# Optimization experiments

Measured on AMD Instinct MI355X. Metric: run time of the kernel, lower is better.

The kernel has to match this reference:

```python
import jax, jax.numpy as jnp
import numpy as np

B, S, D = 2, 2048, 1024
H = 16
DH = D // H  # 64


def setup_inputs() -> dict:
    key = jax.random.key(0)
    ks = jax.random.split(key, 7)
    q = jax.random.normal(ks[0], (B, S, D), dtype=jnp.float32)
    k = jax.random.normal(ks[1], (B, S, D), dtype=jnp.float32)
    v = jax.random.normal(ks[2], (B, S, D), dtype=jnp.float32)
    # torch.rand -> uniform[0,1)
    w_q = jax.random.uniform(ks[3], (D, D), dtype=jnp.float32)
    w_k = jax.random.uniform(ks[4], (DH, D), dtype=jnp.float32)
    w_v = jax.random.uniform(ks[5], (DH, D), dtype=jnp.float32)
    w_out = jax.random.uniform(ks[6], (D, D), dtype=jnp.float32)
    return {"q": q, "k": k, "v": v, "w_q": w_q, "w_k": w_k, "w_v": w_v, "w_out": w_out}


def reference(q, k, v, w_q, w_k, w_v, w_out):
    # F.linear(x, W) = x @ W.T
    qp = jnp.einsum('bsd,ed->bse', q, w_q)          # [B,S,D]
    kp = jnp.einsum('bsd,hd->bsh', k, w_k)          # [B,S,DH] shared K head
    vp = jnp.einsum('bsd,hd->bsh', v, w_v)          # [B,S,DH] shared V head
    qh = qp.reshape(B, S, H, DH).transpose(0, 2, 1, 3)  # [B,H,S,DH]
    scale = 1.0 / jnp.sqrt(jnp.float32(DH))
    scores = jnp.einsum('bhsd,btd->bhst', qh, kp) * scale  # [B,H,S,S]
    attn = jax.nn.softmax(scores, axis=-1)
    out = jnp.einsum('bhst,btd->bhsd', attn, vp)    # [B,H,S,DH]
    out = out.transpose(0, 2, 1, 3).reshape(B, S, D)
    return jnp.einsum('bsd,ed->bse', out, w_out)
```

## Files before the change

kernel.cpp:

```cpp
#include <hip/hip_runtime.h>
#include <hip/hip_bf16.h>
#include <stdint.h>


#define B_   2
#define S_   2048
#define D_   1024
#define H_   16
#define DH_  64
#define MTOT (B_ * S_)
#define NSPL 4

typedef short bf16x8 __attribute__((ext_vector_type(8)));
typedef float f32x4 __attribute__((ext_vector_type(4)));
typedef float f32x16 __attribute__((ext_vector_type(16)));
typedef short short4v __attribute__((ext_vector_type(4)));
typedef unsigned uint4v __attribute__((ext_vector_type(4)));

__device__ __forceinline__ short f2bf(float f) {
  unsigned u = __float_as_uint(f);
  u += 0x7FFF + ((u >> 16) & 1);
  return (short)(u >> 16);
}
__device__ __forceinline__ float bf2f(short h) {
  return __uint_as_float(((unsigned)(unsigned short)h) << 16);
}
struct bfpair { short hi, lo; };
__device__ __forceinline__ bfpair split2(float x) {
  bfpair p;
  p.hi = f2bf(x);
  p.lo = f2bf(x - bf2f(p.hi));
  return p;
}
__device__ __forceinline__ unsigned cvtpk(float lo, float hi) {
  unsigned r;
  asm("v_cvt_pk_bf16_f32 %0, %1, %2" : "=v"(r) : "v"(lo), "v"(hi));
  return r;
}

__device__ __forceinline__ void glds16(const void* g, void* l) {
  __builtin_amdgcn_global_load_lds((const __attribute__((address_space(1))) void*)g,
                                   (__attribute__((address_space(3))) void*)l, 16, 0, 0);
}

__global__ __launch_bounds__(256) void cvt_split(
    const float* __restrict__ q, const float* __restrict__ k, const float* __restrict__ v,
    const float* __restrict__ wq, const float* __restrict__ wk, const float* __restrict__ wv,
    const float* __restrict__ wo,
    short* qhi, short* qlo, short* khi, short* klo, short* vb,
    short* wqh, short* wql, short* wkh, short* wkl, short* wvb,
    short* woh, short* wol) {
  const int U0 = 1048576, U1 = 2097152, U2 = 3145728, U3 = 3407872,
            U4 = 3424256, U5 = 3440640, U6 = 3702784;
  for (int u = blockIdx.x * blockDim.x + threadIdx.x; u < U6; u += gridDim.x * blockDim.x) {
    const float* s; short* dh; short* dl; int r;
    if (u < U0)      { s = q;  dh = qhi; dl = qlo; r = u; }
    else if (u < U1) { s = k;  dh = khi; dl = klo; r = u - U0; }
    else if (u < U2) { s = v;  dh = vb;  dl = nullptr; r = u - U1; }
    else if (u < U3) { s = wq; dh = wqh; dl = wql; r = u - U2; }
    else if (u < U4) { s = wk; dh = wkh; dl = wkl; r = u - U3; }
    else if (u < U5) { s = wv; dh = wvb; dl = nullptr; r = u - U4; }
    else             { s = wo; dh = woh; dl = wol; r = u - U5; }
    float4 x = *(const float4*)(s + (size_t)r * 4);
    bfpair p0 = split2(x.x), p1 = split2(x.y), p2 = split2(x.z), p3 = split2(x.w);
    short4v yh, yl;
    yh.x = p0.hi; yh.y = p1.hi; yh.z = p2.hi; yh.w = p3.hi;
    yl.x = p0.lo; yl.y = p1.lo; yl.z = p2.lo; yl.w = p3.lo;
    *(short4v*)(dh + (size_t)r * 4) = yh;
    if (dl) *(short4v*)(dl + (size_t)r * 4) = yl;
  }
}

template <int NPROD, int MODE>
__global__ __launch_bounds__(256) void gemm3(
    const short* __restrict__ Ah, const short* __restrict__ Al,
    const short* __restrict__ Bh, const short* __restrict__ Bl,
    short* __restrict__ Ch, short* __restrict__ Cl, float* __restrict__ Cf,
    int K, int lda, int ldb, int ldc, float alpha) {
  __shared__ alignas(16) short Ash[4096], Asl[4096], Bsh[4096], Bsl[4096];
  const int tid = threadIdx.x;
  const int lane = tid & 63, w = tid >> 6;
  const int c = lane & 15, g = lane >> 4;
  const int wm = w >> 1, wn = w & 1;
  const int bm = blockIdx.x * 64, bn = blockIdx.y * 64;
  const int sr = lane >> 3;
  const int scs = ((lane & 7) ^ sr) * 8;

  f32x4 acc[2][2] = {};
  for (int k0 = 0; k0 < K; k0 += 64) {
    glds16(Ah + (size_t)(bm + w * 8 + sr) * lda + k0 + scs,      Ash + w * 512);
    glds16(Ah + (size_t)(bm + 32 + w * 8 + sr) * lda + k0 + scs, Ash + 2048 + w * 512);
    glds16(Bh + (size_t)(bn + w * 8 + sr) * ldb + k0 + scs,      Bsh + w * 512);
    glds16(Bh + (size_t)(bn + 32 + w * 8 + sr) * ldb + k0 + scs, Bsh + 2048 + w * 512);
    if constexpr (NPROD == 3) {
      glds16(Al + (size_t)(bm + w * 8 + sr) * lda + k0 + scs,      Asl + w * 512);
      glds16(Al + (size_t)(bm + 32 + w * 8 + sr) * lda + k0 + scs, Asl + 2048 + w * 512);
      glds16(Bl + (size_t)(bn + w * 8 + sr) * ldb + k0 + scs,      Bsl + w * 512);
      glds16(Bl + (size_t)(bn + 32 + w * 8 + sr) * ldb + k0 + scs, Bsl + 2048 + w * 512);
    }
    __syncthreads();
#pragma unroll
    for (int kk = 0; kk < 2; ++kk) {
      bf16x8 ah[2], bh[2], al[2], bl[2];
#pragma unroll
      for (int mt = 0; mt < 2; ++mt) {
        int row = wm * 32 + mt * 16 + c;
        int so = row * 64 + (((kk * 4 + g) ^ (row & 7)) * 8);
        ah[mt] = *(const bf16x8*)(Ash + so);
        if constexpr (NPROD == 3) al[mt] = *(const bf16x8*)(Asl + so);
      }
#pragma unroll
      for (int nt = 0; nt < 2; ++nt) {
        int row = wn * 32 + nt * 16 + c;
        int so = row * 64 + (((kk * 4 + g) ^ (row & 7)) * 8);
        bh[nt] = *(const bf16x8*)(Bsh + so);
        if constexpr (NPROD == 3) bl[nt] = *(const bf16x8*)(Bsl + so);
      }
#pragma unroll
      for (int mt = 0; mt < 2; ++mt)
#pragma unroll
        for (int nt = 0; nt < 2; ++nt) {
          acc[mt][nt] = __builtin_amdgcn_mfma_f32_16x16x32_bf16(ah[mt], bh[nt], acc[mt][nt], 0, 0, 0);
          if constexpr (NPROD == 3) {
            acc[mt][nt] = __builtin_amdgcn_mfma_f32_16x16x32_bf16(ah[mt], bl[nt], acc[mt][nt], 0, 0, 0);
            acc[mt][nt] = __builtin_amdgcn_mfma_f32_16x16x32_bf16(al[mt], bh[nt], acc[mt][nt], 0, 0, 0);
          }
        }
    }
    __syncthreads();
  }
#pragma unroll
  for (int mt = 0; mt < 2; ++mt) {
#pragma unroll
    for (int nt = 0; nt < 2; ++nt) {
#pragma unroll
      for (int r = 0; r < 4; ++r) {
        int m = bm + wm * 32 + mt * 16 + g * 4 + r;
        int n = bn + wn * 32 + nt * 16 + c;
        float val = acc[mt][nt][r] * alpha;
        if constexpr (MODE == 0) {
          bfpair pr = split2(val);
          Ch[(size_t)m * ldc + n] = pr.hi;
          Cl[(size_t)m * ldc + n] = pr.lo;
        } else if constexpr (MODE == 3) {
          Cf[(size_t)m * ldc + n] = val;
        } else if constexpr (MODE == 4) {
          size_t off = (((size_t)(m >> 5) * 4 + (n >> 4)) * 64 +
                        ((m & 31) + 32 * ((n >> 3) & 1))) * 8 + (n & 7);
          bfpair pr = split2(val);
          Ch[off] = pr.hi;
          Cl[off] = pr.lo;
        } else {
          size_t off = ((((size_t)(m >> 5) * 2 + (n >> 5)) * 2 + ((m >> 4) & 1)) * 64 +
                        ((n & 31) + 32 * ((m >> 3) & 1))) * 8 + (m & 7);
          Ch[off] = f2bf(val);
        }
      }
    }
  }
}

__global__ __launch_bounds__(256) void mqa_attn(
    const short* __restrict__ qph, const short* __restrict__ qpl,
    const short* __restrict__ pkh, const short* __restrict__ pkl,
    const short* __restrict__ pv, short* __restrict__ pO, float* __restrict__ pML) {
  const int tid = threadIdx.x;
  const int lane = tid & 63, w = tid >> 6;
  const int j = lane & 31, b5 = lane >> 5;
  const int qt = blockIdx.x, h = blockIdx.y;
  const int b = blockIdx.z >> 2, sp = blockIdx.z & 3;
  const int q0 = qt * 128 + w * 32;
  const int kvbeg = sp * (S_ / NSPL), kvend = kvbeg + S_ / NSPL;

  const size_t qbase = (size_t)(b * S_ + q0 + j) * D_ + h * DH_ + b5 * 8;
  bf16x8 qh[4], ql[4];
#pragma unroll
  for (int m = 0; m < 4; ++m) {
    qh[m] = *(const bf16x8*)(qph + qbase + m * 16);
    ql[m] = *(const bf16x8*)(qpl + qbase + m * 16);
  }

  float mrow = -1.0e30f, lrow = 0.f;
  f32x16 o0 = {}, o1 = {};

  for (int kv0 = kvbeg; kv0 < kvend; kv0 += 32) {
    const size_t tg = (size_t)((b * S_ + kv0) >> 5);
    const short* kb = pkh + tg * 2048 + lane * 8;
    const short* kb2 = pkl + tg * 2048 + lane * 8;
    bf16x8 kh[4], kl[4];
#pragma unroll
    for (int m = 0; m < 4; ++m) {
      kh[m] = *(const bf16x8*)(kb + m * 512);
      kl[m] = *(const bf16x8*)(kb2 + m * 512);
    }
    f32x16 sa = {}, sb = {}, sc2 = {};
#pragma unroll
    for (int m = 0; m < 4; ++m) {
      sa  = __builtin_amdgcn_mfma_f32_32x32x16_bf16(kh[m], qh[m], sa, 0, 0, 0);
      sb  = __builtin_amdgcn_mfma_f32_32x32x16_bf16(kl[m], qh[m], sb, 0, 0, 0);
      sc2 = __builtin_amdgcn_mfma_f32_32x32x16_bf16(kh[m], ql[m], sc2, 0, 0, 0);
    }
    f32x16 s = (sa + sb) + sc2;
    float mx = s[0];
#pragma unroll
    for (int r = 1; r < 16; ++r) mx = fmaxf(mx, s[r]);
    mx = fmaxf(mx, __shfl_xor(mx, 32));
    if (!__all(mx - mrow <= 8.0f)) {
      float mn = fmaxf(mrow, mx);
      float scale = exp2f(mrow - mn);
      mrow = mn;
      lrow *= scale;
      o0 *= scale;
      o1 *= scale;
    }
    float p[16];
#pragma unroll
    for (int r = 0; r < 16; ++r) p[r] = exp2f(s[r] - mrow);
    float rs = (((p[0] + p[1]) + (p[2] + p[3])) + ((p[4] + p[5]) + (p[6] + p[7]))) +
               (((p[8] + p[9]) + (p[10] + p[11])) + ((p[12] + p[13]) + (p[14] + p[15])));
    rs += __shfl_xor(rs, 32);
    lrow += rs;
    auto r0 = __builtin_amdgcn_permlane32_swap(cvtpk(p[0], p[1]),   cvtpk(p[4], p[5]),   false, false);
    auto r1 = __builtin_amdgcn_permlane32_swap(cvtpk(p[2], p[3]),   cvtpk(p[6], p[7]),   false, false);
    auto r2 = __builtin_amdgcn_permlane32_swap(cvtpk(p[8], p[9]),   cvtpk(p[12], p[13]), false, false);
    auto r3 = __builtin_amdgcn_permlane32_swap(cvtpk(p[10], p[11]), cvtpk(p[14], p[15]), false, false);
    union { uint4v u; bf16x8 v; } pa0, pa1;
    pa0.u = (uint4v){r0[0], r1[0], r0[1], r1[1]};
    pa1.u = (uint4v){r2[0], r3[0], r2[1], r3[1]};
    const short* vbp = pv + tg * 2048 + lane * 8;
    bf16x8 va00 = *(const bf16x8*)(vbp);
    bf16x8 va01 = *(const bf16x8*)(vbp + 512);
    bf16x8 va10 = *(const bf16x8*)(vbp + 1024);
    bf16x8 va11 = *(const bf16x8*)(vbp + 1536);
    o0 = __builtin_amdgcn_mfma_f32_32x32x16_bf16(va00, pa0.v, o0, 0, 0, 0);
    o0 = __builtin_amdgcn_mfma_f32_32x32x16_bf16(va01, pa1.v, o0, 0, 0, 0);
    o1 = __builtin_amdgcn_mfma_f32_32x32x16_bf16(va10, pa0.v, o1, 0, 0, 0);
    o1 = __builtin_amdgcn_mfma_f32_32x32x16_bf16(va11, pa1.v, o1, 0, 0, 0);
  }
  const size_t tok = (size_t)(b * S_ + q0 + j);
  const size_t obase = ((size_t)sp * MTOT + tok) * D_ + h * DH_;
#pragma unroll
  for (int r = 0; r < 16; ++r) {
    int dh0 = (r & 3) + 8 * (r >> 2) + 4 * b5;
    pO[obase + dh0] = f2bf(o0[r]);
    pO[obase + 32 + dh0] = f2bf(o1[r]);
  }
  if (b5 == 0) {
    size_t mb = (((size_t)sp * MTOT + tok) * H_ + h) * 2;
    pML[mb] = mrow;
    pML[mb + 1] = lrow;
  }
}

__global__ __launch_bounds__(256) void attn_merge(
    const short* __restrict__ pO, const float* __restrict__ pML,
    short* __restrict__ aoh, short* __restrict__ aol) {
  int qd = blockIdx.x * 256 + threadIdx.x;
  size_t idx = (size_t)qd * 4;
  int tok = (int)(idx >> 10);
  int h = (int)((idx >> 6) & 15);
  float ms[NSPL], ls[NSPL], mm = -1.0e30f;
#pragma unroll
  for (int s = 0; s < NSPL; ++s) {
    size_t mb = (((size_t)s * MTOT + tok) * H_ + h) * 2;
    ms[s] = pML[mb];
    ls[s] = pML[mb + 1];
    mm = fmaxf(mm, ms[s]);
  }
  float num[4] = {}, den = 0.f;
#pragma unroll
  for (int s = 0; s < NSPL; ++s) {
    float e = exp2f(ms[s] - mm);
    den += ls[s] * e;
    short4v o4 = *(const short4v*)(pO + (size_t)s * MTOT * D_ + idx);
    num[0] += bf2f(o4.x) * e;
    num[1] += bf2f(o4.y) * e;
    num[2] += bf2f(o4.z) * e;
    num[3] += bf2f(o4.w) * e;
  }
  float inv = 1.0f / den;
  short4v yh, yl;
  bfpair p0 = split2(num[0] * inv), p1 = split2(num[1] * inv),
         p2 = split2(num[2] * inv), p3 = split2(num[3] * inv);
  yh.x = p0.hi; yh.y = p1.hi; yh.z = p2.hi; yh.w = p3.hi;
  yl.x = p0.lo; yl.y = p1.lo; yl.z = p2.lo; yl.w = p3.lo;
  *(short4v*)(aoh + idx) = yh;
  *(short4v*)(aol + idx) = yl;
}

extern "C" void kernel_launch(void* const* d_in, const int* in_sizes, int n_in,
                              void* d_out, int out_size, void* d_ws, size_t ws_size,
                              hipStream_t stream) {
  const float* q  = (const float*)d_in[0];
  const float* k  = (const float*)d_in[1];
  const float* v  = (const float*)d_in[2];
  const float* wq = (const float*)d_in[3];
  const float* wk = (const float*)d_in[4];
  const float* wv = (const float*)d_in[5];
  const float* wo = (const float*)d_in[6];

  short* p = (short*)d_ws;
  short* qhi = p; p += 4194304;
  short* qlo = p; p += 4194304;
  short* khi = p; p += 4194304;
  short* klo = p; p += 4194304;
  short* vb  = p; p += 4194304;
  short* wqh = p; p += 1048576;
  short* wql = p; p += 1048576;
  short* wkh = p; p += 65536;
  short* wkl = p; p += 65536;
  short* wvb = p; p += 65536;
  short* woh = p; p += 1048576;
  short* wol = p; p += 1048576;
  short* qph = p; p += 4194304;
  short* qpl = p; p += 4194304;
  short* pkh = p; p += 524288;
  short* pkl = p; p += 524288;
  short* pv  = p; p += 524288;
  short* pO  = qhi;
  float* pML = (float*)vb;
  short* aoh = qph;
  short* aol = qpl;

  cvt_split<<<dim3(2048), dim3(256), 0, stream>>>(q, k, v, wq, wk, wv, wo,
      qhi, qlo, khi, klo, vb, wqh, wql, wkh, wkl, wvb, woh, wol);
  gemm3<3, 0><<<dim3(64, 16), dim3(256), 0, stream>>>(qhi, qlo, wqh, wql, qph, qpl,
      nullptr, 1024, 1024, 1024, 1024, 0.125f * 1.44269504f);
  gemm3<3, 4><<<dim3(64, 1), dim3(256), 0, stream>>>(khi, klo, wkh, wkl, pkh, pkl,
      nullptr, 1024, 1024, 1024, 64, 1.0f);
  gemm3<1, 5><<<dim3(64, 1), dim3(256), 0, stream>>>(vb, nullptr, wvb, nullptr, pv,
      nullptr, nullptr, 1024, 1024, 1024, 64, 1.0f);
  mqa_attn<<<dim3(S_ / 128, 16, B_ * NSPL), dim3(256), 0, stream>>>(
      qph, qpl, pkh, pkl, pv, pO, pML);
  attn_merge<<<dim3(MTOT * D_ / 4 / 256), dim3(256), 0, stream>>>(pO, pML, aoh, aol);
  gemm3<3, 3><<<dim3(64, 16), dim3(256), 0, stream>>>(aoh, aol, woh, wol, nullptr,
      nullptr, (float*)d_out, 1024, 1024, 1024, 1024, 1.0f);
}
```

Before: 234.6 us.

## Drop split-KV attention and merge kernel, normalize output in-kernel

```diff
diff --git a/kernel.cpp b/kernel.cpp
--- a/kernel.cpp
+++ b/kernel.cpp
@@ -9,7 +9,6 @@
 #define H_   16
 #define DH_  64
 #define MTOT (B_ * S_)
-#define NSPL 4
 
 typedef short bf16x8 __attribute__((ext_vector_type(8)));
 typedef float f32x4 __attribute__((ext_vector_type(4)));
@@ -163,14 +162,12 @@
 __global__ __launch_bounds__(256) void mqa_attn(
     const short* __restrict__ qph, const short* __restrict__ qpl,
     const short* __restrict__ pkh, const short* __restrict__ pkl,
-    const short* __restrict__ pv, short* __restrict__ pO, float* __restrict__ pML) {
+    const short* __restrict__ pv, short* __restrict__ aoh, short* __restrict__ aol) {
   const int tid = threadIdx.x;
   const int lane = tid & 63, w = tid >> 6;
   const int j = lane & 31, b5 = lane >> 5;
-  const int qt = blockIdx.x, h = blockIdx.y;
-  const int b = blockIdx.z >> 2, sp = blockIdx.z & 3;
+  const int qt = blockIdx.x, h = blockIdx.y, b = blockIdx.z;
   const int q0 = qt * 128 + w * 32;
-  const int kvbeg = sp * (S_ / NSPL), kvend = kvbeg + S_ / NSPL;
 
   const size_t qbase = (size_t)(b * S_ + q0 + j) * D_ + h * DH_ + b5 * 8;
   bf16x8 qh[4], ql[4];
@@ -183,7 +180,7 @@
   float mrow = -1.0e30f, lrow = 0.f;
   f32x16 o0 = {}, o1 = {};
 
-  for (int kv0 = kvbeg; kv0 < kvend; kv0 += 32) {
+  for (int kv0 = 0; kv0 < S_; kv0 += 32) {
     const size_t tg = (size_t)((b * S_ + kv0) >> 5);
     const short* kb = pkh + tg * 2048 + lane * 8;
     const short* kb2 = pkl + tg * 2048 + lane * 8;
@@ -193,14 +190,16 @@
       kh[m] = *(const bf16x8*)(kb + m * 512);
       kl[m] = *(const bf16x8*)(kb2 + m * 512);
     }
-    f32x16 sa = {}, sb = {}, sc2 = {};
-#pragma unroll
-    for (int m = 0; m < 4; ++m) {
-      sa  = __builtin_amdgcn_mfma_f32_32x32x16_bf16(kh[m], qh[m], sa, 0, 0, 0);
-      sb  = __builtin_amdgcn_mfma_f32_32x32x16_bf16(kl[m], qh[m], sb, 0, 0, 0);
-      sc2 = __builtin_amdgcn_mfma_f32_32x32x16_bf16(kh[m], ql[m], sc2, 0, 0, 0);
-    }
-    f32x16 s = (sa + sb) + sc2;
+    f32x16 s = {};
+#pragma unroll
+    for (int m = 0; m < 4; ++m)
+      s = __builtin_amdgcn_mfma_f32_32x32x16_bf16(kh[m], qh[m], s, 0, 0, 0);
+#pragma unroll
+    for (int m = 0; m < 4; ++m)
+      s = __builtin_amdgcn_mfma_f32_32x32x16_bf16(kl[m], qh[m], s, 0, 0, 0);
+#pragma unroll
+    for (int m = 0; m < 4; ++m)
+      s = __builtin_amdgcn_mfma_f32_32x32x16_bf16(kh[m], ql[m], s, 0, 0, 0);
     float mx = s[0];
 #pragma unroll
     for (int r = 1; r < 16; ++r) mx = fmaxf(mx, s[r]);
@@ -237,55 +236,18 @@
     o1 = __builtin_amdgcn_mfma_f32_32x32x16_bf16(va10, pa0.v, o1, 0, 0, 0);
     o1 = __builtin_amdgcn_mfma_f32_32x32x16_bf16(va11, pa1.v, o1, 0, 0, 0);
   }
-  const size_t tok = (size_t)(b * S_ + q0 + j);
-  const size_t obase = ((size_t)sp * MTOT + tok) * D_ + h * DH_;
+  float inv = 1.0f / lrow;
+  const size_t obase = (size_t)(b * S_ + q0 + j) * D_ + h * DH_;
 #pragma unroll
   for (int r = 0; r < 16; ++r) {
     int dh0 = (r & 3) + 8 * (r >> 2) + 4 * b5;
-    pO[obase + dh0] = f2bf(o0[r]);
-    pO[obase + 32 + dh0] = f2bf(o1[r]);
-  }
-  if (b5 == 0) {
-    size_t mb = (((size_t)sp * MTOT + tok) * H_ + h) * 2;
-    pML[mb] = mrow;
-    pML[mb + 1] = lrow;
-  }
-}
-
-__global__ __launch_bounds__(256) void attn_merge(
-    const short* __restrict__ pO, const float* __restrict__ pML,
-    short* __restrict__ aoh, short* __restrict__ aol) {
-  int qd = blockIdx.x * 256 + threadIdx.x;
-  size_t idx = (size_t)qd * 4;
-  int tok = (int)(idx >> 10);
-  int h = (int)((idx >> 6) & 15);
-  float ms[NSPL], ls[NSPL], mm = -1.0e30f;
-#pragma unroll
-  for (int s = 0; s < NSPL; ++s) {
-    size_t mb = (((size_t)s * MTOT + tok) * H_ + h) * 2;
-    ms[s] = pML[mb];
-    ls[s] = pML[mb + 1];
-    mm = fmaxf(mm, ms[s]);
-  }
-  float num[4] = {}, den = 0.f;
-#pragma unroll
-  for (int s = 0; s < NSPL; ++s) {
-    float e = exp2f(ms[s] - mm);
-    den += ls[s] * e;
-    short4v o4 = *(const short4v*)(pO + (size_t)s * MTOT * D_ + idx);
-    num[0] += bf2f(o4.x) * e;
-    num[1] += bf2f(o4.y) * e;
-    num[2] += bf2f(o4.z) * e;
-    num[3] += bf2f(o4.w) * e;
-  }
-  float inv = 1.0f / den;
-  short4v yh, yl;
-  bfpair p0 = split2(num[0] * inv), p1 = split2(num[1] * inv),
-         p2 = split2(num[2] * inv), p3 = split2(num[3] * inv);
-  yh.x = p0.hi; yh.y = p1.hi; yh.z = p2.hi; yh.w = p3.hi;
-  yl.x = p0.lo; yl.y = p1.lo; yl.z = p2.lo; yl.w = p3.lo;
-  *(short4v*)(aoh + idx) = yh;
-  *(short4v*)(aol + idx) = yl;
+    bfpair pr0 = split2(o0[r] * inv);
+    aoh[obase + dh0] = pr0.hi;
+    aol[obase + dh0] = pr0.lo;
+    bfpair pr1 = split2(o1[r] * inv);
+    aoh[obase + 32 + dh0] = pr1.hi;
+    aol[obase + 32 + dh0] = pr1.lo;
+  }
 }
 
 extern "C" void kernel_launch(void* const* d_in, const int* in_sizes, int n_in,
@@ -317,10 +279,8 @@
   short* pkh = p; p += 524288;
   short* pkl = p; p += 524288;
   short* pv  = p; p += 524288;
-  short* pO  = qhi;
-  float* pML = (float*)vb;
-  short* aoh = qph;
-  short* aol = qpl;
+  short* aoh = qhi;
+  short* aol = qlo;
 
   cvt_split<<<dim3(2048), dim3(256), 0, stream>>>(q, k, v, wq, wk, wv, wo,
       qhi, qlo, khi, klo, vb, wqh, wql, wkh, wkl, wvb, woh, wol);
@@ -330,9 +290,8 @@
       nullptr, 1024, 1024, 1024, 64, 1.0f);
   gemm3<1, 5><<<dim3(64, 1), dim3(256), 0, stream>>>(vb, nullptr, wvb, nullptr, pv,
       nullptr, nullptr, 1024, 1024, 1024, 64, 1.0f);
-  mqa_attn<<<dim3(S_ / 128, 16, B_ * NSPL), dim3(256), 0, stream>>>(
-      qph, qpl, pkh, pkl, pv, pO, pML);
-  attn_merge<<<dim3(MTOT * D_ / 4 / 256), dim3(256), 0, stream>>>(pO, pML, aoh, aol);
+  mqa_attn<<<dim3(S_ / 128, 16, B_), dim3(256), 0, stream>>>(
+      qph, qpl, pkh, pkl, pv, aoh, aol);
   gemm3<3, 3><<<dim3(64, 16), dim3(256), 0, stream>>>(aoh, aol, woh, wol, nullptr,
       nullptr, (float*)d_out, 1024, 1024, 1024, 1024, 1.0f);
 }
```

Measured after the change: 220.4 us. 1.06x faster.
